# Optimization experiments

Hardware: AMD Instinct MI355X
Metric: run time of the kernel (lower is better)

## Reference

```python
import jax, jax.numpy as jnp
import numpy as np

N_HEADS = 8
TANH_CLIPPING = 10.0
TEMP = 1.0


def setup_inputs() -> dict:
    key = jax.random.key(0)
    ks = jax.random.split(key, 8)
    B, N, D, CTX = 256, 1000, 128, 130
    embeddings = jax.random.normal(ks[0], (B, N, D), dtype=jnp.float32)
    step_context = jax.random.normal(ks[1], (B, 1, CTX), dtype=jnp.float32)
    mask = jax.random.randint(ks[2], (B, 1, N), 0, 2).astype(bool)
    # ensure at least one feasible node per row (node 0 always feasible)
    mask = mask.at[:, :, 0].set(False)
    W_node = jax.random.normal(ks[3], (D, 3 * D), dtype=jnp.float32) * (1.0 / np.sqrt(D))
    W_fixed = jax.random.normal(ks[4], (D, D), dtype=jnp.float32) * (1.0 / np.sqrt(D))
    W_step = jax.random.normal(ks[5], (CTX, D), dtype=jnp.float32) * (1.0 / np.sqrt(CTX))
    W_out = jax.random.normal(ks[6], (D, D), dtype=jnp.float32) * (1.0 / np.sqrt(D))
    return {"embeddings": embeddings, "step_context": step_context, "mask": mask,
            "W_node": W_node, "W_fixed": W_fixed, "W_step": W_step, "W_out": W_out}


def reference(embeddings, step_context, mask, W_node, W_fixed, W_step, W_out):
    # embeddings: [B, N, D], step_context: [B, 1, D+2], mask: [B, 1, N] (True = infeasible)
    B, N, D = embeddings.shape
    H = N_HEADS
    hd = D // H
    # _precompute: fixed context from graph mean, and K/V/logit_key from node embeddings
    graph_embed = embeddings.mean(axis=1)                       # [B, D]
    fixed_context = graph_embed @ W_fixed                       # [B, D]
    kvl = embeddings @ W_node                                   # [B, N, 3D]
    glimpse_k, glimpse_v, logit_k = jnp.split(kvl, 3, axis=-1)  # each [B, N, D]
    # query = fixed context + projected step context             [B, 1, D]
    query = fixed_context[:, None, :] + step_context @ W_step
    # multi-head glimpse attention (q_len = 1)
    q = query.reshape(B, 1, H, hd).transpose(0, 2, 1, 3)        # [B, H, 1, hd]
    K = glimpse_k.reshape(B, N, H, hd).transpose(0, 2, 1, 3)    # [B, H, N, hd]
    V = glimpse_v.reshape(B, N, H, hd).transpose(0, 2, 1, 3)    # [B, H, N, hd]
    compat = jnp.einsum('bhqd,bhnd->bhqn', q, K) / jnp.sqrt(jnp.float32(hd))
    # mask_inner
    compat = jnp.where(mask[:, None, :, :], -jnp.inf, compat)
    attn = jax.nn.softmax(compat, axis=-1)                      # [B, H, 1, N]
    heads = jnp.einsum('bhqn,bhnd->bhqd', attn, V)              # [B, H, 1, hd]
    glimpse = heads.transpose(0, 2, 1, 3).reshape(B, 1, D) @ W_out  # [B, 1, D]
    # single-head logits against logit_key, tanh-clipped
    logits = jnp.einsum('bqd,bnd->bqn', glimpse, logit_k) / jnp.sqrt(jnp.float32(D))
    logits = jnp.tanh(logits) * TANH_CLIPPING
    # mask_logits
    logits = jnp.where(mask, -jnp.inf, logits)
    log_p = jax.nn.log_softmax(logits / TEMP, axis=-1)          # [B, 1, N]
    return log_p
```

## Files before the change

### kernel.cpp

```cpp
#include <hip/hip_runtime.h>
#include <math.h>

#define NN   1000
#define DD   128
#define CTXN 130
#define NEG_BIG (-1.0e30f)


__global__ __launch_bounds__(1024, 4)
void k1_fused(const float* __restrict__ emb, const float* __restrict__ stepc,
              const void* __restrict__ maskp,
              const float* __restrict__ Wn, const float* __restrict__ Wf,
              const float* __restrict__ Ws,
              float* __restrict__ qpt, int* __restrict__ idxv, int* __restrict__ cntv) {
    const int b = blockIdx.x, t = threadIdx.x;
    const int w = t >> 6, lane = t & 63;
    const float* eb = emb + (size_t)b * (NN * DD);
    __shared__ __align__(16) float S[4096];
    __shared__ float s_mean[128], s_q[128];
    __shared__ int s_misint;
    __shared__ unsigned long long s_bal[16];
    __shared__ int s_woff[16];
    if (t == 0) {
        const unsigned char* mb8 = (const unsigned char*)maskp;
        int any = 0;
        for (int k = 0; k < 64; ++k) any |= mb8[4 * k + 1];
        s_misint = (any == 0) ? 1 : 0;
    }
    {
        const int c4 = t & 31, g = t >> 5;
        float4 a = make_float4(0.f, 0.f, 0.f, 0.f);
        for (int r = g; r < NN; r += 32) {
            const float4 v = *(const float4*)(eb + (size_t)r * DD + c4 * 4);
            a.x += v.x; a.y += v.y; a.z += v.z; a.w += v.w;
        }
        ((float4*)S)[g * 32 + c4] = a;
    }
    __syncthreads();
    if (t < 128) {
        float v = 0.f;
        #pragma unroll
        for (int g = 0; g < 32; ++g) v += S[g * 128 + t];
        s_mean[t] = v * (1.0f / (float)NN);
    }
    __syncthreads();
    {
        const int d = t & 127, p = t >> 7;
        float a = 0.f;
        for (int i = 16 * p; i < 16 * p + 16; ++i)
            a = fmaf(s_mean[i], Wf[i * DD + d], a);
        const float* scb = stepc + (size_t)b * CTXN;
        const int c0 = 16 * p, c1 = (p == 7) ? CTXN : 16 * p + 16;
        for (int c = c0; c < c1; ++c)
            a = fmaf(scb[c], Ws[c * DD + d], a);
        S[p * 128 + d] = a;
    }
    __syncthreads();
    if (t < 128) {
        float v = 0.f;
        #pragma unroll
        for (int p = 0; p < 8; ++p) v += S[p * 128 + t];
        s_q[t] = v;
    }
    __syncthreads();
    {
        const int i = t & 127, h = t >> 7;
        float a = 0.f;
        #pragma unroll
        for (int j = 0; j < 16; ++j)
            a = fmaf(Wn[i * 384 + h * 16 + j], s_q[h * 16 + j], a);
        qpt[(size_t)b * 1024 + h * 128 + i] = a * 0.25f;
    }
    {
        const unsigned char* mk8 = (const unsigned char*)maskp + (size_t)b * NN;
        const int* mk32 = (const int*)maskp + (size_t)b * NN;
        int um = 0;
        if (t < NN) um = s_misint ? (mk32[t] == 0) : (mk8[t] == 0);
        const unsigned long long bal = __ballot(um);
        if (lane == 0) s_bal[w] = bal;
        __syncthreads();
        if (t == 0) {
            int o = 0;
            #pragma unroll
            for (int w2 = 0; w2 < 16; ++w2) {
                s_woff[w2] = o;
                o += (int)__popcll(s_bal[w2]);
            }
            cntv[b] = o;
        }
        __syncthreads();
        if (um) {
            const int pos = s_woff[w] +
                (int)__popcll(bal & ((lane == 0) ? 0ULL : (~0ULL >> (64 - lane))));
            idxv[(size_t)b * 1024 + pos] = t;
        }
    }
}

__global__ __launch_bounds__(512, 4)
void kB_stream(const float* __restrict__ emb, const float* __restrict__ qpt,
               const int* __restrict__ idxv, const int* __restrict__ cntv,
               float* __restrict__ wembp, float* __restrict__ stats) {
    const int b = blockIdx.x >> 3, s = blockIdx.x & 7;
    const int t = threadIdx.x, w = t >> 6, lane = t & 63;
    const int rg = lane >> 4, cl = lane & 15;
    const int cnt = cntv[b];
    const int lo = (s * cnt) >> 3;
    const int hi = ((s + 1) * cnt) >> 3;
    const int nrows = hi - lo;
    const float* eb = emb + (size_t)b * (NN * DD);
    __shared__ __align__(16) float s_qpT[1024];
    __shared__ __align__(16) float s_part[8 * 8 * 132];
    __shared__ float s_sumw[64];
    __shared__ int s_idx[128];
    for (int i = t; i < 1024; i += 512) s_qpT[i] = qpt[(size_t)b * 1024 + i];
    if (t < 128) s_idx[t] = (t < nrows) ? idxv[(size_t)b * 1024 + lo + t] : 0;
    __syncthreads();
    const int h0 = 2 * rg, h1 = 2 * rg + 1;
    const float4 qa0 = *(const float4*)&s_qpT[h0 * 128 + cl * 8];
    const float4 qa1 = *(const float4*)&s_qpT[h0 * 128 + cl * 8 + 4];
    const float4 qb0 = *(const float4*)&s_qpT[h1 * 128 + cl * 8];
    const float4 qb1 = *(const float4*)&s_qpT[h1 * 128 + cl * 8 + 4];
    float4 a0A = make_float4(0.f,0.f,0.f,0.f), a0B = a0A;
    float4 a1A = a0A, a1B = a0A;
    float ps0 = 0.f, ps1 = 0.f;
    const int niter = (nrows + 7) >> 3;
    for (int it = 0; it < niter; ++it) {
        const int rp = it * 8 + w;
        const bool valid = (rp < nrows);
        const int n = s_idx[rp & 127];
        float4 e0 = make_float4(0.f,0.f,0.f,0.f), e1 = e0;
        if (valid) {
            e0 = *(const float4*)(eb + (size_t)n * DD + cl * 8);
            e1 = *(const float4*)(eb + (size_t)n * DD + cl * 8 + 4);
        }
        float c0 = e0.x * qa0.x;
        c0 = fmaf(e0.y, qa0.y, c0); c0 = fmaf(e0.z, qa0.z, c0); c0 = fmaf(e0.w, qa0.w, c0);
        c0 = fmaf(e1.x, qa1.x, c0); c0 = fmaf(e1.y, qa1.y, c0);
        c0 = fmaf(e1.z, qa1.z, c0); c0 = fmaf(e1.w, qa1.w, c0);
        float c1 = e0.x * qb0.x;
        c1 = fmaf(e0.y, qb0.y, c1); c1 = fmaf(e0.z, qb0.z, c1); c1 = fmaf(e0.w, qb0.w, c1);
        c1 = fmaf(e1.x, qb1.x, c1); c1 = fmaf(e1.y, qb1.y, c1);
        c1 = fmaf(e1.z, qb1.z, c1); c1 = fmaf(e1.w, qb1.w, c1);
        c0 += __shfl_xor(c0, 1, 16); c1 += __shfl_xor(c1, 1, 16);
        c0 += __shfl_xor(c0, 2, 16); c1 += __shfl_xor(c1, 2, 16);
        c0 += __shfl_xor(c0, 4, 16); c1 += __shfl_xor(c1, 4, 16);
        c0 += __shfl_xor(c0, 8, 16); c1 += __shfl_xor(c1, 8, 16);
        const float p0 = valid ? expf(fminf(c0, 80.f)) : 0.f;
        const float p1 = valid ? expf(fminf(c1, 80.f)) : 0.f;
        ps0 += p0; ps1 += p1;
        a0A.x = fmaf(p0, e0.x, a0A.x); a0A.y = fmaf(p0, e0.y, a0A.y);
        a0A.z = fmaf(p0, e0.z, a0A.z); a0A.w = fmaf(p0, e0.w, a0A.w);
        a0B.x = fmaf(p0, e1.x, a0B.x); a0B.y = fmaf(p0, e1.y, a0B.y);
        a0B.z = fmaf(p0, e1.z, a0B.z); a0B.w = fmaf(p0, e1.w, a0B.w);
        a1A.x = fmaf(p1, e0.x, a1A.x); a1A.y = fmaf(p1, e0.y, a1A.y);
        a1A.z = fmaf(p1, e0.z, a1A.z); a1A.w = fmaf(p1, e0.w, a1A.w);
        a1B.x = fmaf(p1, e1.x, a1B.x); a1B.y = fmaf(p1, e1.y, a1B.y);
        a1B.z = fmaf(p1, e1.z, a1B.z); a1B.w = fmaf(p1, e1.w, a1B.w);
    }
    *(float4*)&s_part[(w * 8 + h0) * 132 + cl * 8]     = a0A;
    *(float4*)&s_part[(w * 8 + h0) * 132 + cl * 8 + 4] = a0B;
    *(float4*)&s_part[(w * 8 + h1) * 132 + cl * 8]     = a1A;
    *(float4*)&s_part[(w * 8 + h1) * 132 + cl * 8 + 4] = a1B;
    if (cl == 0) { s_sumw[w * 8 + h0] = ps0; s_sumw[w * 8 + h1] = ps1; }
    __syncthreads();
    for (int i = t; i < 1024; i += 512) {
        const int h = i >> 7, c = i & 127;
        float v = 0.f;
        #pragma unroll
        for (int w2 = 0; w2 < 8; ++w2) v += s_part[(w2 * 8 + h) * 132 + c];
        wembp[(size_t)b * 8192 + s * 1024 + i] = v;
    }
    if (t < 8) {
        float v = 0.f;
        #pragma unroll
        for (int w2 = 0; w2 < 8; ++w2) v += s_sumw[w2 * 8 + t];
        stats[(size_t)b * 64 + s * 8 + t] = v;
    }
}

__global__ __launch_bounds__(1024, 4)
void k4_fused(const float* __restrict__ emb, const float* __restrict__ wembp,
              const float* __restrict__ stats,
              const float* __restrict__ Wn, const float* __restrict__ Wo,
              const int* __restrict__ idxv, const int* __restrict__ cntv,
              float* __restrict__ out) {
    const int b = blockIdx.x, t = threadIdx.x;
    const int w = t >> 6, lane = t & 63;
    const int rg = lane >> 4, cl = lane & 15;
    const float* eb = emb + (size_t)b * (NN * DD);
    __shared__ float s_dinv[8];
    __shared__ float s_wemb[8 * 130];
    __shared__ __align__(16) float s_red[1024];
    __shared__ float s_h[128], s_gl[128], s_g2[128];
    __shared__ float s_logits[1000];
    __shared__ int s_idxf[1024];
    __shared__ float s_r2[32];
    __shared__ float s_lse;
    const int cnt = cntv[b];
    if (t < NN) s_logits[t] = NEG_BIG;
    s_idxf[t] = (t < cnt) ? idxv[(size_t)b * 1024 + t] : 0;
    if (t < 8) {
        float den = 0.f;
        #pragma unroll
        for (int ss = 0; ss < 8; ++ss) den += stats[(size_t)b * 64 + ss * 8 + t];
        s_dinv[t] = 1.0f / den;
    }
    __syncthreads();
    {
        const int h = t >> 7, i = t & 127;
        float v = 0.f;
        #pragma unroll
        for (int ss = 0; ss < 8; ++ss)
            v += wembp[(size_t)b * 8192 + ss * 1024 + t];
        s_wemb[h * 130 + i] = v * s_dinv[h];
    }
    __syncthreads();
    {
        const int j = t & 127, p = t >> 7;
        float a = 0.f;
        for (int i = 16 * p; i < 16 * p + 16; ++i)
            a = fmaf(Wn[i * 384 + 128 + j], s_wemb[(j >> 4) * 130 + i], a);
        s_red[p * 128 + j] = a;
    }
    __syncthreads();
    if (t < 128) {
        float v = 0.f;
        #pragma unroll
        for (int p = 0; p < 8; ++p) v += s_red[p * 128 + t];
        s_h[t] = v;
    }
    __syncthreads();
    {
        const int d = t & 127, p = t >> 7;
        float a = 0.f;
        for (int j = 16 * p; j < 16 * p + 16; ++j)
            a = fmaf(s_h[j], Wo[j * DD + d], a);
        s_red[p * 128 + d] = a;
    }
    __syncthreads();
    if (t < 128) {
        float v = 0.f;
        #pragma unroll
        for (int p = 0; p < 8; ++p) v += s_red[p * 128 + t];
        s_gl[t] = v;
    }
    __syncthreads();
    {
        const int i = t & 127, p = t >> 7;
        float a = 0.f;
        for (int d = 16 * p; d < 16 * p + 16; ++d)
            a = fmaf(Wn[i * 384 + 256 + d], s_gl[d], a);
        s_red[p * 128 + i] = a;
    }
    __syncthreads();
    if (t < 128) {
        float v = 0.f;
        #pragma unroll
        for (int p = 0; p < 8; ++p) v += s_red[p * 128 + t];
        s_g2[t] = v * 0.08838834764831845f;
    }
    __syncthreads();
    {
        const float4 ga = *(const float4*)&s_g2[cl * 8];
        const float4 gb = *(const float4*)&s_g2[cl * 8 + 4];
        const int niterL = (cnt + 63) >> 6;
        for (int it = 0; it < niterL; ++it) {
            const int pos = it * 64 + w * 4 + rg;
            const bool valid = (pos < cnt);
            const int n = s_idxf[pos & 1023];
            float a = 0.f;
            if (valid) {
                const float4 e0 = *(const float4*)(eb + (size_t)n * DD + cl * 8);
                const float4 e1 = *(const float4*)(eb + (size_t)n * DD + cl * 8 + 4);
                a = e0.x * ga.x;
                a = fmaf(e0.y, ga.y, a);
                a = fmaf(e0.z, ga.z, a);
                a = fmaf(e0.w, ga.w, a);
                a = fmaf(e1.x, gb.x, a);
                a = fmaf(e1.y, gb.y, a);
                a = fmaf(e1.z, gb.z, a);
                a = fmaf(e1.w, gb.w, a);
            }
            a += __shfl_xor(a, 1, 16);
            a += __shfl_xor(a, 2, 16);
            a += __shfl_xor(a, 4, 16);
            a += __shfl_xor(a, 8, 16);
            if (cl == 0 && valid)
                s_logits[n] = 10.0f * tanhf(a);
        }
    }
    __syncthreads();
    {
        float sum = (t < NN) ? expf(s_logits[t]) : 0.f;
        #pragma unroll
        for (int o = 32; o; o >>= 1) sum += __shfl_xor(sum, o, 64);
        if (lane == 0) s_r2[w] = sum;
        __syncthreads();
        if (t == 0) {
            float ss = 0.f;
            #pragma unroll
            for (int i = 0; i < 16; ++i) ss += s_r2[i];
            s_lse = logf(ss);
        }
        __syncthreads();
        if (t < NN) out[(size_t)b * NN + t] = s_logits[t] - s_lse;
    }
}

extern "C" void kernel_launch(void* const* d_in, const int* in_sizes, int n_in,
                              void* d_out, int out_size, void* d_ws, size_t ws_size,
                              hipStream_t stream) {
    const float* emb   = (const float*)d_in[0];
    const float* stepc = (const float*)d_in[1];
    const void*  mask  = (const void*)d_in[2];
    const float* Wn = (const float*)d_in[3];
    const float* Wf = (const float*)d_in[4];
    const float* Ws = (const float*)d_in[5];
    const float* Wo = (const float*)d_in[6];
    float* out = (float*)d_out;
    const int B = in_sizes[0] / (NN * DD);

    float* wsf = (float*)d_ws;
    const size_t n_qpt   = (size_t)B * 1024;
    const size_t n_wembp = (size_t)B * 8192;
    const size_t n_stats = (size_t)B * 64;
    const size_t n_idx   = (size_t)B * 1024;

    float* qpt   = wsf;
    float* wembp = qpt + n_qpt;
    float* stats = wembp + n_wembp;
    int*   idxv  = (int*)(stats + n_stats);
    int*   cntv  = idxv + n_idx;

    k1_fused <<<B,     1024, 0, stream>>>(emb, stepc, mask, Wn, Wf, Ws, qpt, idxv, cntv);
    kB_stream<<<B * 8, 512,  0, stream>>>(emb, qpt, idxv, cntv, wembp, stats);
    k4_fused <<<B,     1024, 0, stream>>>(emb, wembp, stats, Wn, Wo, idxv, cntv, out);
}
```

Baseline: 81.37 us.

## Project V inside streaming kernel, write per-split head partials instead of weighted embeddings

The V projection (multiply of the attention-weighted embeddings by the V slice of W_node) moves from the final kernel into each of the 8 split blocks of the streaming kernel. Each split now writes 128 head partials instead of 1024 weighted-embedding floats, so the workspace traffic between kernels shrinks eightfold. This relies on linearity: the final kernel sums the split partials and applies the per-head softmax normalisation afterward. The cost is that the W_node projection is now done 8 times per batch (once per split), adding redundant FMAs and weight reads to the streaming kernel.

New measurement: 80.40 us. Within noise of the previous version (-1.2%).

```diff
diff --git a/kernel.cpp b/kernel.cpp
--- a/kernel.cpp
+++ b/kernel.cpp
@@ -99,8 +99,9 @@
 
 __global__ __launch_bounds__(512, 4)
 void kB_stream(const float* __restrict__ emb, const float* __restrict__ qpt,
+               const float* __restrict__ Wn,
                const int* __restrict__ idxv, const int* __restrict__ cntv,
-               float* __restrict__ wembp, float* __restrict__ stats) {
+               float* __restrict__ headsp, float* __restrict__ stats) {
     const int b = blockIdx.x >> 3, s = blockIdx.x & 7;
     const int t = threadIdx.x, w = t >> 6, lane = t & 63;
     const int rg = lane >> 4, cl = lane & 15;
@@ -164,13 +165,36 @@
     *(float4*)&s_part[(w * 8 + h1) * 132 + cl * 8 + 4] = a1B;
     if (cl == 0) { s_sumw[w * 8 + h0] = ps0; s_sumw[w * 8 + h1] = ps1; }
     __syncthreads();
-    for (int i = t; i < 1024; i += 512) {
-        const int h = i >> 7, c = i & 127;
-        float v = 0.f;
-        #pragma unroll
-        for (int w2 = 0; w2 < 8; ++w2) v += s_part[(w2 * 8 + h) * 132 + c];
-        wembp[(size_t)b * 8192 + s * 1024 + i] = v;
-    }
+    float vres0, vres1;
+    {
+        const int i0 = t, i1 = t + 512;
+        const int hA = i0 >> 7, cA = i0 & 127;
+        const int hB = i1 >> 7, cB = i1 & 127;
+        float v0 = 0.f, v1 = 0.f;
+        #pragma unroll
+        for (int w2 = 0; w2 < 8; ++w2) {
+            v0 += s_part[(w2 * 8 + hA) * 132 + cA];
+            v1 += s_part[(w2 * 8 + hB) * 132 + cB];
+        }
+        vres0 = v0; vres1 = v1;
+    }
+    __syncthreads();
+    s_part[t]       = vres0;
+    s_part[t + 512] = vres1;
+    __syncthreads();
+    {
+        const int j = t & 127, p = t >> 7;
+        const int h = j >> 4;
+        float a = 0.f;
+        for (int i = 32 * p; i < 32 * p + 32; ++i)
+            a = fmaf(Wn[i * 384 + 128 + j], s_part[h * 128 + i], a);
+        s_part[1024 + p * 128 + j] = a;
+    }
+    __syncthreads();
+    if (t < 128)
+        headsp[(size_t)b * 1024 + s * 128 + t] =
+            s_part[1024 + t] + s_part[1024 + 128 + t] +
+            s_part[1024 + 256 + t] + s_part[1024 + 384 + t];
     if (t < 8) {
         float v = 0.f;
         #pragma unroll
@@ -180,7 +204,7 @@
 }
 
 __global__ __launch_bounds__(1024, 4)
-void k4_fused(const float* __restrict__ emb, const float* __restrict__ wembp,
+void k4_fused(const float* __restrict__ emb, const float* __restrict__ headsp,
               const float* __restrict__ stats,
               const float* __restrict__ Wn, const float* __restrict__ Wo,
               const int* __restrict__ idxv, const int* __restrict__ cntv,
@@ -190,7 +214,6 @@
     const int rg = lane >> 4, cl = lane & 15;
     const float* eb = emb + (size_t)b * (NN * DD);
     __shared__ float s_dinv[8];
-    __shared__ float s_wemb[8 * 130];
     __shared__ __align__(16) float s_red[1024];
     __shared__ float s_h[128], s_gl[128], s_g2[128];
     __shared__ float s_logits[1000];
@@ -207,28 +230,11 @@
         s_dinv[t] = 1.0f / den;
     }
     __syncthreads();
-    {
-        const int h = t >> 7, i = t & 127;
-        float v = 0.f;
-        #pragma unroll
-        for (int ss = 0; ss < 8; ++ss)
-            v += wembp[(size_t)b * 8192 + ss * 1024 + t];
-        s_wemb[h * 130 + i] = v * s_dinv[h];
-    }
-    __syncthreads();
-    {
-        const int j = t & 127, p = t >> 7;
-        float a = 0.f;
-        for (int i = 16 * p; i < 16 * p + 16; ++i)
-            a = fmaf(Wn[i * 384 + 128 + j], s_wemb[(j >> 4) * 130 + i], a);
-        s_red[p * 128 + j] = a;
-    }
-    __syncthreads();
-    if (t < 128) {
-        float v = 0.f;
-        #pragma unroll
-        for (int p = 0; p < 8; ++p) v += s_red[p * 128 + t];
-        s_h[t] = v;
+    if (t < 128) {
+        float v = 0.f;
+        #pragma unroll
+        for (int ss = 0; ss < 8; ++ss) v += headsp[(size_t)b * 1024 + ss * 128 + t];
+        s_h[t] = v * s_dinv[t >> 4];
     }
     __syncthreads();
     {
@@ -323,17 +329,17 @@
 
     float* wsf = (float*)d_ws;
     const size_t n_qpt   = (size_t)B * 1024;
-    const size_t n_wembp = (size_t)B * 8192;
+    const size_t n_hp    = (size_t)B * 1024;
     const size_t n_stats = (size_t)B * 64;
     const size_t n_idx   = (size_t)B * 1024;
 
-    float* qpt   = wsf;
-    float* wembp = qpt + n_qpt;
-    float* stats = wembp + n_wembp;
-    int*   idxv  = (int*)(stats + n_stats);
-    int*   cntv  = idxv + n_idx;
+    float* qpt    = wsf;
+    float* headsp = qpt + n_qpt;
+    float* stats  = headsp + n_hp;
+    int*   idxv   = (int*)(stats + n_stats);
+    int*   cntv   = idxv + n_idx;
 
     k1_fused <<<B,     1024, 0, stream>>>(emb, stepc, mask, Wn, Wf, Ws, qpt, idxv, cntv);
-    kB_stream<<<B * 8, 512,  0, stream>>>(emb, qpt, idxv, cntv, wembp, stats);
-    k4_fused <<<B,     1024, 0, stream>>>(emb, wembp, stats, Wn, Wo, idxv, cntv, out);
+    kB_stream<<<B * 8, 512,  0, stream>>>(emb, qpt, Wn, idxv, cntv, headsp, stats);
+    k4_fused <<<B,     1024, 0, stream>>>(emb, headsp, stats, Wn, Wo, idxv, cntv, out);
 }
```
